# Optimization experiments

Measured on AMD Instinct MI355X. Metric: run time of the kernel, lower is better.

## Reference

```python
import jax, jax.numpy as jnp
import numpy as np

K = 20  # neighbors (includes self, as PyG knn(x,x,k) does)
B, P = 8, 2048


def _knn_idx(pts, k):
    # pts: [P, D] -> [P, k] indices of k nearest (self included, dist 0)
    sq = jnp.sum(pts * pts, axis=-1)
    dist = sq[:, None] + sq[None, :] - 2.0 * (pts @ pts.T)
    return jax.lax.top_k(-dist, k)[1]


def _edge_conv(x, W, b, k):
    # DynamicEdgeConv with single-Linear nn and max aggregation.
    # x: [B,P,D]; W: [C, 2D]; message = Lin([x_i, x_j - x_i])
    D = x.shape[-1]
    Wa, Wb = W[:, :D], W[:, D:]
    idx = jax.vmap(lambda p: _knn_idx(p, k))(x)                 # [B,P,k]
    nb = jax.vmap(lambda xb, ib: xb[ib])(x, idx)                # [B,P,k,D]
    msg = (x @ Wa.T)[:, :, None, :] + (nb - x[:, :, None, :]) @ Wb.T + b
    return jnp.max(msg, axis=2)                                 # [B,P,C]


def _lin(h, W, b):
    return h @ W.T + b


def setup_inputs() -> dict:
    key = jax.random.key(0)
    ks = jax.random.split(key, 16)
    N = B * P

    def w(k_, shape):
        fan_in = shape[-1]
        return (jax.random.normal(k_, shape, dtype=jnp.float32) / np.sqrt(fan_in)).astype(jnp.float32)

    inp = {
        "pos": jax.random.normal(ks[0], (N, 3), dtype=jnp.float32),
        "x": jax.random.normal(ks[1], (N, 3), dtype=jnp.float32),
        "features": jax.random.normal(ks[2], (N, 1344), dtype=jnp.float32),
        "batch": (jnp.arange(N) // P).astype(jnp.int64) if jax.config.jax_enable_x64 else (jnp.arange(N) // P).astype(jnp.int32),
        # filter_conv: Conv2d(1344,128,1) == Linear 1344->128
        "Wf": w(ks[3], (128, 1344)), "bf": jnp.zeros((128,), jnp.float32),
        # edge MLPs (single Linear each, plain_last)
        "W1": w(ks[4], (64, 2 * 134)), "b1": jnp.zeros((64,), jnp.float32),
        "W2": w(ks[5], (128, 2 * 64)), "b2": jnp.zeros((128,), jnp.float32),
        "W3": w(ks[6], (256, 2 * 128)), "b3": jnp.zeros((256,), jnp.float32),
        # fc1: Linear 576->1024
        "Wfc1": w(ks[7], (1024, 576)), "bfc1": jnp.zeros((1024,), jnp.float32),
        # fc2: 1024->512->256->23 with ReLU on hidden layers
        "Wfa": w(ks[8], (512, 1024)), "bfa": jnp.zeros((512,), jnp.float32),
        "Wfb": w(ks[9], (256, 512)), "bfb": jnp.zeros((256,), jnp.float32),
        "Wfc": w(ks[10], (23, 256)), "bfc": jnp.zeros((23,), jnp.float32),
    }
    return inp


def reference(pos, x, features, batch, Wf, bf, W1, b1, W2, b2, W3, b3,
              Wfc1, bfc1, Wfa, bfa, Wfb, bfb, Wfc, bfc):
    N = pos.shape[0]
    nB = int(batch[-1]) + 1
    nP = N // nB

    feats = _lin(features, Wf, bf)                              # [N,128] (1x1 conv)
    h0 = jnp.concatenate([pos, x, feats], axis=1).reshape(nB, nP, -1)  # [B,P,134]

    x1 = _edge_conv(h0, W1, b1, K)                              # [B,P,64]
    x2 = _edge_conv(x1, W2, b2, K)                              # [B,P,128]
    x3 = _edge_conv(x2, W3, b3, K)                              # [B,P,256]

    cat = jnp.concatenate([x1, x2, x3, feats.reshape(nB, nP, -1)], axis=-1)  # [B,P,576]
    h = _lin(cat, Wfc1, bfc1)                                   # [B,P,1024]
    g = jnp.max(h, axis=1)                                      # global_max_pool -> [B,1024]
    g = jax.nn.relu(_lin(g, Wfa, bfa))
    g = jax.nn.relu(_lin(g, Wfb, bfb))
    g = _lin(g, Wfc, bfc)
    return jax.nn.log_softmax(g, axis=1)                        # [B,23]
```

## Files before the change

### kernel.cpp

```cpp
#include <hip/hip_runtime.h>
#include <math.h>

#define PPB 2048
#define NBATCH 8
#define KNN 20

typedef __attribute__((ext_vector_type(8))) short short8;
typedef __attribute__((ext_vector_type(8))) __bf16 bf16x8;
typedef __attribute__((ext_vector_type(4))) float f32x4;

__global__ __launch_bounds__(256) void gemm_feats_kernel(
    const float* __restrict__ X, const float* __restrict__ W,
    float* __restrict__ fpart, int N) {
  const int KC = 336;
  int kc = blockIdx.z;
  const float* Xp = X + kc * KC;
  const float* Wp = W + kc * KC;
  float* Y = fpart + (size_t)kc * N * 128;
  __shared__ float Xs[8][132];
  __shared__ float Ws[8][132];
  int t = threadIdx.x;
  int tx = t & 15, ty = t >> 4;
  int i0 = blockIdx.y * 128;
  float acc[8][8];
#pragma unroll
  for (int r = 0; r < 8; ++r)
#pragma unroll
    for (int n = 0; n < 8; ++n) acc[r][n] = 0.f;

  for (int k0 = 0; k0 < KC; k0 += 8) {
#pragma unroll
    for (int p = 0; p < 4; ++p) {
      int e = t + p * 256, r = e >> 3, c = e & 7, k = k0 + c;
      Xs[c][r] = Xp[(size_t)(i0 + r) * 1344 + k];
      Ws[c][r] = Wp[(size_t)r * 1344 + k];
    }
    __syncthreads();
#pragma unroll
    for (int k = 0; k < 8; ++k) {
      float4 a0 = *(const float4*)&Xs[k][ty * 8];
      float4 a1 = *(const float4*)&Xs[k][ty * 8 + 4];
      float a[8] = {a0.x, a0.y, a0.z, a0.w, a1.x, a1.y, a1.z, a1.w};
      float4 b0 = *(const float4*)&Ws[k][tx * 8];
      float4 b1 = *(const float4*)&Ws[k][tx * 8 + 4];
      float bb[8] = {b0.x, b0.y, b0.z, b0.w, b1.x, b1.y, b1.z, b1.w};
#pragma unroll
      for (int r = 0; r < 8; ++r)
#pragma unroll
        for (int n = 0; n < 8; ++n) acc[r][n] += a[r] * bb[n];
    }
    __syncthreads();
  }
#pragma unroll
  for (int r = 0; r < 8; ++r) {
    size_t row = (size_t)(i0 + ty * 8 + r) * 128 + tx * 8;
#pragma unroll
    for (int n4 = 0; n4 < 2; ++n4) {
      float4 o;
      o.x = acc[r][n4 * 4 + 0]; o.y = acc[r][n4 * 4 + 1];
      o.z = acc[r][n4 * 4 + 2]; o.w = acc[r][n4 * 4 + 3];
      *(float4*)&Y[row + n4 * 4] = o;
    }
  }
}

__global__ __launch_bounds__(256) void reduce_feats_kernel(
    const float* __restrict__ fpart, const float* __restrict__ bias,
    float* __restrict__ catbuf, int N) {
  int e = blockIdx.x * 256 + threadIdx.x;
  size_t NP = (size_t)N * 128;
  int i = e >> 7, m = e & 127;
  float s = bias[m] + fpart[e] + fpart[NP + e] + fpart[2 * NP + e] + fpart[3 * NP + e];
  catbuf[(size_t)i * 576 + 448 + m] = s;
}

__global__ __launch_bounds__(256) void edge_gemm_kernel(
    const float* __restrict__ X, int ldx, int D,
    const float* __restrict__ W, int ldw, int M,
    float* __restrict__ A, float* __restrict__ Pb) {
  __shared__ float Xs[16][68];
  __shared__ float Ws[16][68];
  int t = threadIdx.x, tx = t & 15, ty = t >> 4;
  int nHalf = M >> 6;
  int mt = blockIdx.x;
  int is_b = (mt >= nHalf) ? 1 : 0;
  int m0 = (is_b ? mt - nHalf : mt) << 6;
  int koff = is_b ? D : 0;
  float* __restrict__ out = is_b ? Pb : A;
  int i0 = blockIdx.y * 64;
  float acc[4][4];
#pragma unroll
  for (int r = 0; r < 4; ++r)
#pragma unroll
    for (int n = 0; n < 4; ++n) acc[r][n] = 0.f;

  for (int k0 = 0; k0 < D; k0 += 16) {
#pragma unroll
    for (int p = 0; p < 4; ++p) {
      int e = t + p * 256, r = e >> 4, c = e & 15, k = k0 + c;
      Xs[c][r] = (k < D) ? X[(size_t)(i0 + r) * ldx + k] : 0.f;
      Ws[c][r] = (k < D) ? W[(size_t)(m0 + r) * ldw + koff + k] : 0.f;
    }
    __syncthreads();
#pragma unroll
    for (int kk = 0; kk < 16; ++kk) {
      float4 a4 = *(const float4*)&Xs[kk][ty * 4];
      float4 b4 = *(const float4*)&Ws[kk][tx * 4];
      float a[4] = {a4.x, a4.y, a4.z, a4.w};
      float bb[4] = {b4.x, b4.y, b4.z, b4.w};
#pragma unroll
      for (int r = 0; r < 4; ++r)
#pragma unroll
        for (int n = 0; n < 4; ++n) acc[r][n] += a[r] * bb[n];
    }
    __syncthreads();
  }
#pragma unroll
  for (int r = 0; r < 4; ++r) {
    float4 o;
    o.x = acc[r][0]; o.y = acc[r][1]; o.z = acc[r][2]; o.w = acc[r][3];
    *(float4*)&out[(size_t)(i0 + ty * 4 + r) * M + m0 + tx * 4] = o;
  }
}

__global__ __launch_bounds__(256) void cast_bf16_kernel(
    const float* __restrict__ src, unsigned short* __restrict__ dst, int n) {
  int e4 = (blockIdx.x * 256 + threadIdx.x) * 4;
  if (e4 >= n) return;
  float4 v = *(const float4*)&src[e4];
  ushort4 o;
  unsigned int u;
  u = __float_as_uint(v.x); o.x = (unsigned short)((u + 0x7fff + ((u >> 16) & 1)) >> 16);
  u = __float_as_uint(v.y); o.y = (unsigned short)((u + 0x7fff + ((u >> 16) & 1)) >> 16);
  u = __float_as_uint(v.z); o.z = (unsigned short)((u + 0x7fff + ((u >> 16) & 1)) >> 16);
  u = __float_as_uint(v.w); o.w = (unsigned short)((u + 0x7fff + ((u >> 16) & 1)) >> 16);
  *(ushort4*)&dst[e4] = o;
}

__global__ __launch_bounds__(256) void cast_hl_kernel(
    const float* __restrict__ X, int ldx, int D, int Kp,
    unsigned short* __restrict__ hi, unsigned short* __restrict__ lo) {
  int i = blockIdx.x;
  for (int k = threadIdx.x; k < Kp; k += 256) {
    float x = (k < D) ? X[(size_t)i * ldx + k] : 0.f;
    unsigned int u = __float_as_uint(x);
    unsigned short h = (unsigned short)((u + 0x7fff + ((u >> 16) & 1)) >> 16);
    float hf = __uint_as_float((unsigned int)h << 16);
    float r = x - hf;
    unsigned int v = __float_as_uint(r);
    unsigned short l16 = (unsigned short)((v + 0x7fff + ((v >> 16) & 1)) >> 16);
    hi[(size_t)i * Kp + k] = h;
    lo[(size_t)i * Kp + k] = l16;
  }
}

template <int KP>
__global__ __launch_bounds__(256) void dist_gemm2_kernel(
    const unsigned short* __restrict__ Xhi,
    const unsigned short* __restrict__ Xlo,
    const float* __restrict__ sq,
    float* __restrict__ dist, int zBase) {
  __shared__ unsigned short Ah[128][40];
  __shared__ unsigned short Al[128][40];
  __shared__ unsigned short Bh[64][40];
  __shared__ unsigned short Bl[64][40];
  int t = threadIdx.x;
  int l = t & 63, w = t >> 6;
  int z = blockIdx.z;
  size_t bbase = (size_t)(zBase + z) * PPB;
  int c0 = blockIdx.x * 64, q0 = blockIdx.y * 128;

  f32x4 acc[2][4];
#pragma unroll
  for (int qs = 0; qs < 2; ++qs)
#pragma unroll
    for (int cc = 0; cc < 4; ++cc) acc[qs][cc] = (f32x4){0.f, 0.f, 0.f, 0.f};

  for (int k0 = 0; k0 < KP; k0 += 32) {
    short8 sa[2][2];
#pragma unroll
    for (int p = 0; p < 2; ++p) {
      int e = t + p * 256, row = e >> 2, kg = e & 3;
      sa[p][0] = *(const short8*)&Xhi[(bbase + q0 + row) * KP + k0 + kg * 8];
      sa[p][1] = *(const short8*)&Xlo[(bbase + q0 + row) * KP + k0 + kg * 8];
    }
    int brow = t >> 2, bkg = t & 3;
    short8 sb0 = *(const short8*)&Xhi[(bbase + c0 + brow) * KP + k0 + bkg * 8];
    short8 sb1 = *(const short8*)&Xlo[(bbase + c0 + brow) * KP + k0 + bkg * 8];
    __syncthreads();
#pragma unroll
    for (int p = 0; p < 2; ++p) {
      int e = t + p * 256, row = e >> 2, kg = e & 3;
      *(short8*)&Ah[row][kg * 8] = sa[p][0];
      *(short8*)&Al[row][kg * 8] = sa[p][1];
    }
    *(short8*)&Bh[brow][bkg * 8] = sb0;
    *(short8*)&Bl[brow][bkg * 8] = sb1;
    __syncthreads();

    bf16x8 ah[2], al[2], bh[4], bl[4];
#pragma unroll
    for (int qs = 0; qs < 2; ++qs) {
      int row = w * 32 + qs * 16 + (l & 15);
      ah[qs] = __builtin_bit_cast(bf16x8, *(const short8*)&Ah[row][(l >> 4) * 8]);
      al[qs] = __builtin_bit_cast(bf16x8, *(const short8*)&Al[row][(l >> 4) * 8]);
    }
#pragma unroll
    for (int cc = 0; cc < 4; ++cc) {
      bh[cc] = __builtin_bit_cast(bf16x8, *(const short8*)&Bh[cc * 16 + (l & 15)][(l >> 4) * 8]);
      bl[cc] = __builtin_bit_cast(bf16x8, *(const short8*)&Bl[cc * 16 + (l & 15)][(l >> 4) * 8]);
    }
#pragma unroll
    for (int qs = 0; qs < 2; ++qs)
#pragma unroll
      for (int cc = 0; cc < 4; ++cc) {
        acc[qs][cc] = __builtin_amdgcn_mfma_f32_16x16x32_bf16(ah[qs], bh[cc], acc[qs][cc], 0, 0, 0);
        acc[qs][cc] = __builtin_amdgcn_mfma_f32_16x16x32_bf16(ah[qs], bl[cc], acc[qs][cc], 0, 0, 0);
        acc[qs][cc] = __builtin_amdgcn_mfma_f32_16x16x32_bf16(al[qs], bh[cc], acc[qs][cc], 0, 0, 0);
      }
  }
  float* dz = dist + (size_t)z * PPB * PPB;
#pragma unroll
  for (int cc = 0; cc < 4; ++cc) {
    int j = c0 + cc * 16 + (l & 15);
    float sqj = sq[bbase + j];
#pragma unroll
    for (int qs = 0; qs < 2; ++qs) {
      int qb = q0 + w * 32 + qs * 16 + (l >> 4) * 4;
#pragma unroll
      for (int r = 0; r < 4; ++r)
        dz[(size_t)(qb + r) * PPB + j] = sqj - 2.f * acc[qs][cc][r];
    }
  }
}

__global__ __launch_bounds__(256) void knn_sel3_kernel(
    const float* __restrict__ dist, int zBase, int* __restrict__ idx) {
  int z = blockIdx.y;
  int b = zBase + z;
  int q = blockIdx.x * 4 + (threadIdx.x >> 6);
  int lane = threadIdx.x & 63;
  const float* row = dist + ((size_t)z * PPB + q) * PPB + lane * 32;

  float v[32];
#pragma unroll
  for (int m4 = 0; m4 < 8; ++m4) {
    float4 f = *(const float4*)&row[m4 * 4];
    v[m4 * 4 + 0] = f.x; v[m4 * 4 + 1] = f.y;
    v[m4 * 4 + 2] = f.z; v[m4 * 4 + 3] = f.w;
  }
  float gv[8]; int gi[8];
#pragma unroll
  for (int g = 0; g < 8; ++g) {
    float bv = v[g * 4]; int bi = 0;
    if (v[g * 4 + 1] < bv) { bv = v[g * 4 + 1]; bi = 1; }
    if (v[g * 4 + 2] < bv) { bv = v[g * 4 + 2]; bi = 2; }
    if (v[g * 4 + 3] < bv) { bv = v[g * 4 + 3]; bi = 3; }
    gv[g] = bv; gi[g] = g * 4 + bi;
  }
  float lv = gv[0]; int lm = gi[0];
#pragma unroll
  for (int g = 1; g < 8; ++g)
    if (gv[g] < lv) { lv = gv[g]; lm = gi[g]; }
  unsigned u0 = __float_as_uint(lv);
  unsigned lk = u0 ^ (((int)u0 >> 31) | 0x80000000u);

  unsigned rm = 0;
#pragma unroll
  for (int s = 0; s < KNN; ++s) {
    unsigned bk = lk;
    int bj = lane * 32 + lm;
#pragma unroll
    for (int o = 1; o < 64; o <<= 1) {
      unsigned ok = __shfl_xor(bk, o);
      int oj = __shfl_xor(bj, o);
      if (ok < bk || (ok == bk && oj < bj)) { bk = ok; bj = oj; }
    }
    if (lane == 0)
      idx[((size_t)b * PPB + q) * KNN + s] = b * PPB + bj;
    if ((bj >> 5) == lane) {
      int m = bj & 31;
      rm |= (1u << m);
      int g = m >> 2;
      float e0 = v[0], e1 = v[1], e2 = v[2], e3 = v[3];
#pragma unroll
      for (int gg = 1; gg < 8; ++gg) {
        bool sel = (g == gg);
        e0 = sel ? v[gg * 4 + 0] : e0;
        e1 = sel ? v[gg * 4 + 1] : e1;
        e2 = sel ? v[gg * 4 + 2] : e2;
        e3 = sel ? v[gg * 4 + 3] : e3;
      }
      unsigned gm = (rm >> (g * 4)) & 15u;
      if (gm & 1u) e0 = 1e38f;
      if (gm & 2u) e1 = 1e38f;
      if (gm & 4u) e2 = 1e38f;
      if (gm & 8u) e3 = 1e38f;
      float nv = e0; int ni = 0;
      if (e1 < nv) { nv = e1; ni = 1; }
      if (e2 < nv) { nv = e2; ni = 2; }
      if (e3 < nv) { nv = e3; ni = 3; }
#pragma unroll
      for (int gg = 0; gg < 8; ++gg)
        if (g == gg) { gv[gg] = nv; gi[gg] = gg * 4 + ni; }
      lv = gv[0]; lm = gi[0];
#pragma unroll
      for (int gg = 1; gg < 8; ++gg)
        if (gv[gg] < lv) { lv = gv[gg]; lm = gi[gg]; }
      unsigned u = __float_as_uint(lv);
      lk = u ^ (((int)u >> 31) | 0x80000000u);
    }
  }
}

__global__ __launch_bounds__(256) void fc1max_mfma_kernel(
    const unsigned short* __restrict__ Xb, const unsigned short* __restrict__ Wb,
    const float* __restrict__ bias, float* __restrict__ partial) {
  __shared__ unsigned short Xs[64][40];
  __shared__ unsigned short Ws[64][40];
  __shared__ float red[4][64];
  int t = threadIdx.x;
  int l = t & 63, w = t >> 6;
  int b = blockIdx.z, pt = blockIdx.y;
  int i0 = b * PPB + pt * 64;
  int m0 = blockIdx.x * 64;
  int r_st = t >> 2;
  int c_st = (t & 3) * 8;

  f32x4 acc[4];
#pragma unroll
  for (int g = 0; g < 4; ++g) acc[g] = (f32x4){0.f, 0.f, 0.f, 0.f};

  for (int k0 = 0; k0 < 576; k0 += 32) {
    short8 xv = *(const short8*)&Xb[(size_t)(i0 + r_st) * 576 + k0 + c_st];
    short8 wv = *(const short8*)&Wb[(size_t)(m0 + r_st) * 576 + k0 + c_st];
    __syncthreads();
    *(short8*)&Xs[r_st][c_st] = xv;
    *(short8*)&Ws[r_st][c_st] = wv;
    __syncthreads();
    short8 ar = *(const short8*)&Xs[16 * w + (l & 15)][(l >> 4) * 8];
    bf16x8 av = __builtin_bit_cast(bf16x8, ar);
#pragma unroll
    for (int g = 0; g < 4; ++g) {
      short8 br = *(const short8*)&Ws[g * 16 + (l & 15)][(l >> 4) * 8];
      bf16x8 bv = __builtin_bit_cast(bf16x8, br);
      acc[g] = __builtin_amdgcn_mfma_f32_16x16x32_bf16(av, bv, acc[g], 0, 0, 0);
    }
  }
  float pm[4];
#pragma unroll
  for (int g = 0; g < 4; ++g) {
    float m = fmaxf(fmaxf(acc[g][0], acc[g][1]), fmaxf(acc[g][2], acc[g][3]));
    m = fmaxf(m, __shfl_xor(m, 16));
    m = fmaxf(m, __shfl_xor(m, 32));
    pm[g] = m;
  }
  if (l < 16) {
#pragma unroll
    for (int g = 0; g < 4; ++g) red[w][g * 16 + l] = pm[g];
  }
  __syncthreads();
  if (t < 64) {
    float mx = fmaxf(fmaxf(red[0][t], red[1][t]), fmaxf(red[2][t], red[3][t]));
    partial[((size_t)b * (PPB / 64) + pt) * 1024 + m0 + t] = mx + bias[m0 + t];
  }
}

__global__ __launch_bounds__(256) void gmax_kernel(
    const float* __restrict__ partial, float* __restrict__ g) {
  int b = blockIdx.y;
  int m = blockIdx.x * 256 + threadIdx.x;
  float mx = -INFINITY;
  for (int pt = 0; pt < PPB / 64; ++pt)
    mx = fmaxf(mx, partial[((size_t)b * (PPB / 64) + pt) * 1024 + m]);
  g[b * 1024 + m] = mx;
}

__global__ __launch_bounds__(192) void h0_kernel(
    const float* __restrict__ pos, const float* __restrict__ xin,
    const float* __restrict__ catbuf, float* __restrict__ h0) {
  int i = blockIdx.x;
  int d = threadIdx.x;
  if (d < 3)        h0[(size_t)i * 134 + d] = pos[i * 3 + d];
  else if (d < 6)   h0[(size_t)i * 134 + d] = xin[i * 3 + d - 3];
  else if (d < 134) h0[(size_t)i * 134 + d] = catbuf[(size_t)i * 576 + 448 + (d - 6)];
}

__global__ __launch_bounds__(64) void sq_kernel(
    const float* __restrict__ X, int ldx, int D, float* __restrict__ sq) {
  int i = blockIdx.x;
  int t = threadIdx.x;
  float s = 0.f;
  for (int k = t; k < D; k += 64) {
    float v = X[(size_t)i * ldx + k];
    s += v * v;
  }
  for (int off = 32; off > 0; off >>= 1) s += __shfl_down(s, off);
  if (t == 0) sq[i] = s;
}

__global__ __launch_bounds__(256) void edge_out_kernel(
    const float* __restrict__ A, const float* __restrict__ Pb, int M,
    const float* __restrict__ bias, const int* __restrict__ idx,
    float* __restrict__ Y, int ldy) {
  int i = blockIdx.x;
  int t = threadIdx.x;
  __shared__ int nbs[KNN];
  if (t < KNN) nbs[t] = idx[(size_t)i * KNN + t];
  __syncthreads();
  for (int m = t; m < M; m += 256) {
    float mx = -INFINITY;
#pragma unroll
    for (int kk = 0; kk < KNN; ++kk)
      mx = fmaxf(mx, Pb[(size_t)nbs[kk] * M + m]);
    Y[(size_t)i * ldy + m] = A[(size_t)i * M + m] + bias[m] - Pb[(size_t)i * M + m] + mx;
  }
}

__global__ __launch_bounds__(256) void mlp2_kernel(
    const float* __restrict__ X, const float* __restrict__ W,
    const float* __restrict__ bias, float* __restrict__ Y,
    int D, int M, int do_relu) {
  int b = blockIdx.y;
  int m = blockIdx.x * 4 + (threadIdx.x >> 6);
  int lane = threadIdx.x & 63;
  const float* xr = X + (size_t)b * D;
  const float* wr = W + (size_t)m * D;
  float s = 0.f;
  for (int k = lane * 4; k < D; k += 256) {
    float4 xv = *(const float4*)&xr[k];
    float4 wv = *(const float4*)&wr[k];
    s += xv.x * wv.x + xv.y * wv.y + xv.z * wv.z + xv.w * wv.w;
  }
#pragma unroll
  for (int o = 32; o > 0; o >>= 1) s += __shfl_down(s, o);
  if (lane == 0) {
    s += bias[m];
    if (do_relu) s = fmaxf(s, 0.f);
    Y[(size_t)b * M + m] = s;
  }
}

__global__ __launch_bounds__(256) void final2_kernel(
    const float* __restrict__ X, const float* __restrict__ W,
    const float* __restrict__ bias, float* __restrict__ out) {
  int b = blockIdx.x;
  int w = threadIdx.x >> 6, lane = threadIdx.x & 63;
  __shared__ float lg[23];
  const float* xr = X + (size_t)b * 256;
  float4 xv = *(const float4*)&xr[lane * 4];
  for (int c = w; c < 23; c += 4) {
    const float* wr = W + (size_t)c * 256;
    float4 wv = *(const float4*)&wr[lane * 4];
    float s = xv.x * wv.x + xv.y * wv.y + xv.z * wv.z + xv.w * wv.w;
#pragma unroll
    for (int o = 32; o > 0; o >>= 1) s += __shfl_down(s, o);
    if (lane == 0) lg[c] = s + bias[c];
  }
  __syncthreads();
  if (threadIdx.x == 0) {
    float mx = lg[0];
    for (int c = 1; c < 23; ++c) mx = fmaxf(mx, lg[c]);
    float s = 0.f;
    for (int c = 0; c < 23; ++c) s += expf(lg[c] - mx);
    float lse = mx + logf(s);
    for (int c = 0; c < 23; ++c) out[b * 23 + c] = lg[c] - lse;
  }
}


extern "C" void kernel_launch(void* const* d_in, const int* in_sizes, int n_in,
                              void* d_out, int out_size, void* d_ws, size_t ws_size,
                              hipStream_t stream) {
  const float* pos      = (const float*)d_in[0];
  const float* xin      = (const float*)d_in[1];
  const float* features = (const float*)d_in[2];
  const float* Wf   = (const float*)d_in[4];
  const float* bf   = (const float*)d_in[5];
  const float* W1   = (const float*)d_in[6];
  const float* b1   = (const float*)d_in[7];
  const float* W2   = (const float*)d_in[8];
  const float* b2   = (const float*)d_in[9];
  const float* W3   = (const float*)d_in[10];
  const float* b3   = (const float*)d_in[11];
  const float* Wfc1 = (const float*)d_in[12];
  const float* bfc1 = (const float*)d_in[13];
  const float* Wfa  = (const float*)d_in[14];
  const float* bfa  = (const float*)d_in[15];
  const float* Wfb  = (const float*)d_in[16];
  const float* bfb  = (const float*)d_in[17];
  const float* Wfc  = (const float*)d_in[18];
  const float* bfc  = (const float*)d_in[19];
  float* out = (float*)d_out;

  const int N = in_sizes[0] / 3;

  char* base = (char*)d_ws;
  size_t off = 0;
  auto alloc = [&](size_t bytes) {
    void* p = base + off;
    off += (bytes + 255) & ~(size_t)255;
    return p;
  };
  float* catbuf  = (float*)alloc((size_t)N * 576 * 4);
  float* h0      = (float*)alloc((size_t)N * 134 * 4);
  float* Abuf    = (float*)alloc((size_t)N * 256 * 4);
  float* Pbbuf   = (float*)alloc((size_t)N * 256 * 4);
  unsigned short* Xhi = (unsigned short*)alloc((size_t)N * 160 * 2);
  unsigned short* Xlo = (unsigned short*)alloc((size_t)N * 160 * 2);
  float* sqbuf   = (float*)alloc((size_t)N * 4);
  int*   idxbuf  = (int*)  alloc((size_t)N * KNN * 4);
  float* partial = (float*)alloc((size_t)NBATCH * (PPB / 64) * 1024 * 4);
  float* g       = (float*)alloc((size_t)NBATCH * 1024 * 4);
  float* ga      = (float*)alloc((size_t)NBATCH * 512 * 4);
  float* gb      = (float*)alloc((size_t)NBATCH * 256 * 4);

  const size_t distBatch = (size_t)PPB * PPB * 4;
  int nz;
  float* dist;
  if (ws_size >= off + 4 * distBatch + 256) {
    nz = 4;  dist = (float*)alloc(4 * distBatch);
  } else {
    nz = 2;  dist = Abuf;
  }

  float* fpart = Abuf;
  unsigned short* catb16 = (unsigned short*)Abuf;
  unsigned short* Wb16   = (unsigned short*)h0;

  gemm_feats_kernel<<<dim3(1, N / 128, 4), 256, 0, stream>>>(features, Wf, fpart, N);
  reduce_feats_kernel<<<(N * 128) / 256, 256, 0, stream>>>(fpart, bf, catbuf, N);

  h0_kernel<<<N, 192, 0, stream>>>(pos, xin, catbuf, h0);

  struct Layer {
    const float* Xin; int ldx; int D; int Kp;
    const float* W; int ldw;
    const float* bias; int M;
    float* Yout;
  };
  Layer L[3] = {
      {h0,          134, 134, 160, W1, 268, b1,  64, catbuf + 0},
      {catbuf + 0,  576,  64,  64, W2, 128, b2, 128, catbuf + 64},
      {catbuf + 64, 576, 128, 128, W3, 256, b3, 256, catbuf + 192},
  };

  for (int l = 0; l < 3; ++l) {
    sq_kernel<<<N, 64, 0, stream>>>(L[l].Xin, L[l].ldx, L[l].D, sqbuf);
    cast_hl_kernel<<<N, 256, 0, stream>>>(L[l].Xin, L[l].ldx, L[l].D, L[l].Kp, Xhi, Xlo);
    for (int p = 0; p < NBATCH; p += nz) {
      if (L[l].Kp == 160)
        dist_gemm2_kernel<160><<<dim3(PPB / 64, PPB / 128, nz), 256, 0, stream>>>(
            Xhi, Xlo, sqbuf, dist, p);
      else if (L[l].Kp == 64)
        dist_gemm2_kernel<64><<<dim3(PPB / 64, PPB / 128, nz), 256, 0, stream>>>(
            Xhi, Xlo, sqbuf, dist, p);
      else
        dist_gemm2_kernel<128><<<dim3(PPB / 64, PPB / 128, nz), 256, 0, stream>>>(
            Xhi, Xlo, sqbuf, dist, p);
      knn_sel3_kernel<<<dim3(PPB / 4, nz), 256, 0, stream>>>(dist, p, idxbuf);
    }
    edge_gemm_kernel<<<dim3((2 * L[l].M) / 64, N / 64), 256, 0, stream>>>(
        L[l].Xin, L[l].ldx, L[l].D, L[l].W, L[l].ldw, L[l].M, Abuf, Pbbuf);
    edge_out_kernel<<<N, 256, 0, stream>>>(
        Abuf, Pbbuf, L[l].M, L[l].bias, idxbuf, L[l].Yout, 576);
  }

  cast_bf16_kernel<<<(N * 576) / 1024, 256, 0, stream>>>(catbuf, catb16, N * 576);
  cast_bf16_kernel<<<(1024 * 576) / 1024, 256, 0, stream>>>(Wfc1, Wb16, 1024 * 576);

  fc1max_mfma_kernel<<<dim3(1024 / 64, PPB / 64, NBATCH), 256, 0, stream>>>(
      catb16, Wb16, bfc1, partial);
  gmax_kernel<<<dim3(1024 / 256, NBATCH), 256, 0, stream>>>(partial, g);

  mlp2_kernel<<<dim3(512 / 4, NBATCH), 256, 0, stream>>>(g,  Wfa, bfa, ga, 1024, 512, 1);
  mlp2_kernel<<<dim3(256 / 4, NBATCH), 256, 0, stream>>>(ga, Wfb, bfb, gb, 512, 256, 1);
  final2_kernel<<<NBATCH, 256, 0, stream>>>(gb, Wfc, bfc, out);
}
```

Baseline: 733.3 us.

## Fuse distance GEMM and top-k selection into one kernel using LDS rows

Replaces the separate distance GEMM (which wrote full 2048x2048 distance matrices to global memory) and the kNN selection kernel with a single kernel. Each 512-thread block computes 16 query rows against all 2048 candidates with MFMA, keeps the distances in a 128KB LDS tile, and then runs the wave-level top-k directly from LDS using packed 64-bit key/index shuffles. This removes the global round trip of the distance matrices and the batch loop of launches. In exchange, the B operand is loaded straight from global memory without LDS staging, and the large LDS footprint limits occupancy to one block per CU.

```diff
diff --git a/kernel.cpp b/kernel.cpp
--- a/kernel.cpp
+++ b/kernel.cpp
@@ -155,160 +155,119 @@
 }
 
 template <int KP>
-__global__ __launch_bounds__(256) void dist_gemm2_kernel(
+__global__ __launch_bounds__(512) void knn_fused_kernel(
     const unsigned short* __restrict__ Xhi,
     const unsigned short* __restrict__ Xlo,
     const float* __restrict__ sq,
-    float* __restrict__ dist, int zBase) {
-  __shared__ unsigned short Ah[128][40];
-  __shared__ unsigned short Al[128][40];
-  __shared__ unsigned short Bh[64][40];
-  __shared__ unsigned short Bl[64][40];
+    int* __restrict__ idx) {
+  __shared__ float dls[16][PPB];
   int t = threadIdx.x;
   int l = t & 63, w = t >> 6;
-  int z = blockIdx.z;
-  size_t bbase = (size_t)(zBase + z) * PPB;
-  int c0 = blockIdx.x * 64, q0 = blockIdx.y * 128;
-
-  f32x4 acc[2][4];
-#pragma unroll
-  for (int qs = 0; qs < 2; ++qs)
-#pragma unroll
-    for (int cc = 0; cc < 4; ++cc) acc[qs][cc] = (f32x4){0.f, 0.f, 0.f, 0.f};
-
-  for (int k0 = 0; k0 < KP; k0 += 32) {
-    short8 sa[2][2];
-#pragma unroll
-    for (int p = 0; p < 2; ++p) {
-      int e = t + p * 256, row = e >> 2, kg = e & 3;
-      sa[p][0] = *(const short8*)&Xhi[(bbase + q0 + row) * KP + k0 + kg * 8];
-      sa[p][1] = *(const short8*)&Xlo[(bbase + q0 + row) * KP + k0 + kg * 8];
-    }
-    int brow = t >> 2, bkg = t & 3;
-    short8 sb0 = *(const short8*)&Xhi[(bbase + c0 + brow) * KP + k0 + bkg * 8];
-    short8 sb1 = *(const short8*)&Xlo[(bbase + c0 + brow) * KP + k0 + bkg * 8];
-    __syncthreads();
-#pragma unroll
-    for (int p = 0; p < 2; ++p) {
-      int e = t + p * 256, row = e >> 2, kg = e & 3;
-      *(short8*)&Ah[row][kg * 8] = sa[p][0];
-      *(short8*)&Al[row][kg * 8] = sa[p][1];
-    }
-    *(short8*)&Bh[brow][bkg * 8] = sb0;
-    *(short8*)&Bl[brow][bkg * 8] = sb1;
-    __syncthreads();
-
-    bf16x8 ah[2], al[2], bh[4], bl[4];
-#pragma unroll
-    for (int qs = 0; qs < 2; ++qs) {
-      int row = w * 32 + qs * 16 + (l & 15);
-      ah[qs] = __builtin_bit_cast(bf16x8, *(const short8*)&Ah[row][(l >> 4) * 8]);
-      al[qs] = __builtin_bit_cast(bf16x8, *(const short8*)&Al[row][(l >> 4) * 8]);
-    }
-#pragma unroll
-    for (int cc = 0; cc < 4; ++cc) {
-      bh[cc] = __builtin_bit_cast(bf16x8, *(const short8*)&Bh[cc * 16 + (l & 15)][(l >> 4) * 8]);
-      bl[cc] = __builtin_bit_cast(bf16x8, *(const short8*)&Bl[cc * 16 + (l & 15)][(l >> 4) * 8]);
-    }
-#pragma unroll
-    for (int qs = 0; qs < 2; ++qs)
-#pragma unroll
-      for (int cc = 0; cc < 4; ++cc) {
-        acc[qs][cc] = __builtin_amdgcn_mfma_f32_16x16x32_bf16(ah[qs], bh[cc], acc[qs][cc], 0, 0, 0);
-        acc[qs][cc] = __builtin_amdgcn_mfma_f32_16x16x32_bf16(ah[qs], bl[cc], acc[qs][cc], 0, 0, 0);
-        acc[qs][cc] = __builtin_amdgcn_mfma_f32_16x16x32_bf16(al[qs], bh[cc], acc[qs][cc], 0, 0, 0);
+  int z = blockIdx.y;
+  size_t bbase = (size_t)z * PPB;
+  int q0 = blockIdx.x * 16;
+  int c0 = w * 256;
+
+  {
+    f32x4 acc[16];
+#pragma unroll
+    for (int ct = 0; ct < 16; ++ct) acc[ct] = (f32x4){0.f, 0.f, 0.f, 0.f};
+
+    int ar = l & 15, ks = (l >> 4) * 8;
+    for (int k0 = 0; k0 < KP; k0 += 32) {
+      bf16x8 a_hi = __builtin_bit_cast(bf16x8,
+          *(const short8*)&Xhi[(bbase + q0 + ar) * KP + k0 + ks]);
+      bf16x8 a_lo = __builtin_bit_cast(bf16x8,
+          *(const short8*)&Xlo[(bbase + q0 + ar) * KP + k0 + ks]);
+#pragma unroll
+      for (int ct = 0; ct < 16; ++ct) {
+        bf16x8 b_hi = __builtin_bit_cast(bf16x8,
+            *(const short8*)&Xhi[(bbase + c0 + ct * 16 + ar) * KP + k0 + ks]);
+        bf16x8 b_lo = __builtin_bit_cast(bf16x8,
+            *(const short8*)&Xlo[(bbase + c0 + ct * 16 + ar) * KP + k0 + ks]);
+        acc[ct] = __builtin_amdgcn_mfma_f32_16x16x32_bf16(a_hi, b_hi, acc[ct], 0, 0, 0);
+        acc[ct] = __builtin_amdgcn_mfma_f32_16x16x32_bf16(a_hi, b_lo, acc[ct], 0, 0, 0);
+        acc[ct] = __builtin_amdgcn_mfma_f32_16x16x32_bf16(a_lo, b_hi, acc[ct], 0, 0, 0);
       }
-  }
-  float* dz = dist + (size_t)z * PPB * PPB;
-#pragma unroll
-  for (int cc = 0; cc < 4; ++cc) {
-    int j = c0 + cc * 16 + (l & 15);
-    float sqj = sq[bbase + j];
-#pragma unroll
-    for (int qs = 0; qs < 2; ++qs) {
-      int qb = q0 + w * 32 + qs * 16 + (l >> 4) * 4;
+    }
+    int qr = (l >> 4) * 4;
+#pragma unroll
+    for (int ct = 0; ct < 16; ++ct) {
+      int col = c0 + ct * 16 + (l & 15);
+      float sqj = sq[bbase + col];
 #pragma unroll
       for (int r = 0; r < 4; ++r)
-        dz[(size_t)(qb + r) * PPB + j] = sqj - 2.f * acc[qs][cc][r];
-    }
-  }
-}
-
-__global__ __launch_bounds__(256) void knn_sel3_kernel(
-    const float* __restrict__ dist, int zBase, int* __restrict__ idx) {
-  int z = blockIdx.y;
-  int b = zBase + z;
-  int q = blockIdx.x * 4 + (threadIdx.x >> 6);
-  int lane = threadIdx.x & 63;
-  const float* row = dist + ((size_t)z * PPB + q) * PPB + lane * 32;
-
-  float v[32];
-#pragma unroll
-  for (int m4 = 0; m4 < 8; ++m4) {
-    float4 f = *(const float4*)&row[m4 * 4];
-    v[m4 * 4 + 0] = f.x; v[m4 * 4 + 1] = f.y;
-    v[m4 * 4 + 2] = f.z; v[m4 * 4 + 3] = f.w;
-  }
-  float gv[8]; int gi[8];
-#pragma unroll
-  for (int g = 0; g < 8; ++g) {
-    float bv = v[g * 4]; int bi = 0;
-    if (v[g * 4 + 1] < bv) { bv = v[g * 4 + 1]; bi = 1; }
-    if (v[g * 4 + 2] < bv) { bv = v[g * 4 + 2]; bi = 2; }
-    if (v[g * 4 + 3] < bv) { bv = v[g * 4 + 3]; bi = 3; }
-    gv[g] = bv; gi[g] = g * 4 + bi;
-  }
-  float lv = gv[0]; int lm = gi[0];
-#pragma unroll
-  for (int g = 1; g < 8; ++g)
-    if (gv[g] < lv) { lv = gv[g]; lm = gi[g]; }
-  unsigned u0 = __float_as_uint(lv);
-  unsigned lk = u0 ^ (((int)u0 >> 31) | 0x80000000u);
-
-  unsigned rm = 0;
-#pragma unroll
-  for (int s = 0; s < KNN; ++s) {
-    unsigned bk = lk;
-    int bj = lane * 32 + lm;
-#pragma unroll
-    for (int o = 1; o < 64; o <<= 1) {
-      unsigned ok = __shfl_xor(bk, o);
-      int oj = __shfl_xor(bj, o);
-      if (ok < bk || (ok == bk && oj < bj)) { bk = ok; bj = oj; }
-    }
-    if (lane == 0)
-      idx[((size_t)b * PPB + q) * KNN + s] = b * PPB + bj;
-    if ((bj >> 5) == lane) {
-      int m = bj & 31;
-      rm |= (1u << m);
-      int g = m >> 2;
-      float e0 = v[0], e1 = v[1], e2 = v[2], e3 = v[3];
-#pragma unroll
-      for (int gg = 1; gg < 8; ++gg) {
-        bool sel = (g == gg);
-        e0 = sel ? v[gg * 4 + 0] : e0;
-        e1 = sel ? v[gg * 4 + 1] : e1;
-        e2 = sel ? v[gg * 4 + 2] : e2;
-        e3 = sel ? v[gg * 4 + 3] : e3;
+        dls[qr + r][col] = sqj - 2.f * acc[ct][r];
+    }
+  }
+  __syncthreads();
+
+  for (int rr = 0; rr < 2; ++rr) {
+    int qrow = w * 2 + rr;
+    const float* row = &dls[qrow][0];
+
+    float gv[8]; int gi[8];
+#pragma unroll
+    for (int g = 0; g < 8; ++g) {
+      float e0 = row[(g * 4 + 0) * 64 + l];
+      float e1 = row[(g * 4 + 1) * 64 + l];
+      float e2 = row[(g * 4 + 2) * 64 + l];
+      float e3 = row[(g * 4 + 3) * 64 + l];
+      float bv = e0; int bi = 0;
+      if (e1 < bv) { bv = e1; bi = 1; }
+      if (e2 < bv) { bv = e2; bi = 2; }
+      if (e3 < bv) { bv = e3; bi = 3; }
+      gv[g] = bv; gi[g] = g * 4 + bi;
+    }
+    float lv = gv[0]; int lm = gi[0];
+#pragma unroll
+    for (int g = 1; g < 8; ++g)
+      if (gv[g] < lv) { lv = gv[g]; lm = gi[g]; }
+    unsigned u0 = __float_as_uint(lv);
+    unsigned k0v = u0 ^ (((int)u0 >> 31) | 0x80000000u);
+    unsigned long long LP =
+        ((unsigned long long)k0v << 32) | (unsigned)(lm * 64 + l);
+
+    unsigned rm = 0;
+#pragma unroll
+    for (int s = 0; s < KNN; ++s) {
+      unsigned long long p = LP;
+#pragma unroll
+      for (int o = 1; o < 64; o <<= 1) {
+        unsigned long long q = __shfl_xor(p, o);
+        if (q < p) p = q;
       }
-      unsigned gm = (rm >> (g * 4)) & 15u;
-      if (gm & 1u) e0 = 1e38f;
-      if (gm & 2u) e1 = 1e38f;
-      if (gm & 4u) e2 = 1e38f;
-      if (gm & 8u) e3 = 1e38f;
-      float nv = e0; int ni = 0;
-      if (e1 < nv) { nv = e1; ni = 1; }
-      if (e2 < nv) { nv = e2; ni = 2; }
-      if (e3 < nv) { nv = e3; ni = 3; }
-#pragma unroll
-      for (int gg = 0; gg < 8; ++gg)
-        if (g == gg) { gv[gg] = nv; gi[gg] = gg * 4 + ni; }
-      lv = gv[0]; lm = gi[0];
-#pragma unroll
-      for (int gg = 1; gg < 8; ++gg)
-        if (gv[gg] < lv) { lv = gv[gg]; lm = gi[gg]; }
-      unsigned u = __float_as_uint(lv);
-      lk = u ^ (((int)u >> 31) | 0x80000000u);
+      unsigned j = (unsigned)p;
+      if (l == 0)
+        idx[((size_t)(bbase + q0 + qrow)) * KNN + s] = (int)(bbase + j);
+      if ((j & 63u) == (unsigned)l) {
+        int m = (int)(j >> 6);
+        rm |= (1u << m);
+        int g = m >> 2;
+        float e0 = row[(g * 4 + 0) * 64 + l];
+        float e1 = row[(g * 4 + 1) * 64 + l];
+        float e2 = row[(g * 4 + 2) * 64 + l];
+        float e3 = row[(g * 4 + 3) * 64 + l];
+        unsigned gm = (rm >> (g * 4)) & 15u;
+        if (gm & 1u) e0 = 1e38f;
+        if (gm & 2u) e1 = 1e38f;
+        if (gm & 4u) e2 = 1e38f;
+        if (gm & 8u) e3 = 1e38f;
+        float nv = e0; int ni = 0;
+        if (e1 < nv) { nv = e1; ni = 1; }
+        if (e2 < nv) { nv = e2; ni = 2; }
+        if (e3 < nv) { nv = e3; ni = 3; }
+#pragma unroll
+        for (int gg = 0; gg < 8; ++gg)
+          if (g == gg) { gv[gg] = nv; gi[gg] = gg * 4 + ni; }
+        float lv2 = gv[0]; int lm2 = gi[0];
+#pragma unroll
+        for (int gg = 1; gg < 8; ++gg)
+          if (gv[gg] < lv2) { lv2 = gv[gg]; lm2 = gi[gg]; }
+        unsigned u = __float_as_uint(lv2);
+        unsigned k = u ^ (((int)u >> 31) | 0x80000000u);
+        LP = ((unsigned long long)k << 32) | (unsigned)(lm2 * 64 + l);
+      }
     }
   }
 }
@@ -514,15 +473,7 @@
   float* g       = (float*)alloc((size_t)NBATCH * 1024 * 4);
   float* ga      = (float*)alloc((size_t)NBATCH * 512 * 4);
   float* gb      = (float*)alloc((size_t)NBATCH * 256 * 4);
-
-  const size_t distBatch = (size_t)PPB * PPB * 4;
-  int nz;
-  float* dist;
-  if (ws_size >= off + 4 * distBatch + 256) {
-    nz = 4;  dist = (float*)alloc(4 * distBatch);
-  } else {
-    nz = 2;  dist = Abuf;
-  }
+  (void)ws_size;
 
   float* fpart = Abuf;
   unsigned short* catb16 = (unsigned short*)Abuf;
@@ -548,18 +499,15 @@
   for (int l = 0; l < 3; ++l) {
     sq_kernel<<<N, 64, 0, stream>>>(L[l].Xin, L[l].ldx, L[l].D, sqbuf);
     cast_hl_kernel<<<N, 256, 0, stream>>>(L[l].Xin, L[l].ldx, L[l].D, L[l].Kp, Xhi, Xlo);
-    for (int p = 0; p < NBATCH; p += nz) {
-      if (L[l].Kp == 160)
-        dist_gemm2_kernel<160><<<dim3(PPB / 64, PPB / 128, nz), 256, 0, stream>>>(
-            Xhi, Xlo, sqbuf, dist, p);
-      else if (L[l].Kp == 64)
-        dist_gemm2_kernel<64><<<dim3(PPB / 64, PPB / 128, nz), 256, 0, stream>>>(
-            Xhi, Xlo, sqbuf, dist, p);
-      else
-        dist_gemm2_kernel<128><<<dim3(PPB / 64, PPB / 128, nz), 256, 0, stream>>>(
-            Xhi, Xlo, sqbuf, dist, p);
-      knn_sel3_kernel<<<dim3(PPB / 4, nz), 256, 0, stream>>>(dist, p, idxbuf);
-    }
+    if (L[l].Kp == 160)
+      knn_fused_kernel<160><<<dim3(PPB / 16, NBATCH), 512, 0, stream>>>(
+          Xhi, Xlo, sqbuf, idxbuf);
+    else if (L[l].Kp == 64)
+      knn_fused_kernel<64><<<dim3(PPB / 16, NBATCH), 512, 0, stream>>>(
+          Xhi, Xlo, sqbuf, idxbuf);
+    else
+      knn_fused_kernel<128><<<dim3(PPB / 16, NBATCH), 512, 0, stream>>>(
+          Xhi, Xlo, sqbuf, idxbuf);
     edge_gemm_kernel<<<dim3((2 * L[l].M) / 64, N / 64), 256, 0, stream>>>(
         L[l].Xin, L[l].ldx, L[l].D, L[l].W, L[l].ldw, L[l].M, Abuf, Pbbuf);
     edge_out_kernel<<<N, 256, 0, stream>>>(
```

Result: slower. 957.8 us (+30.6%).
